# Kernel tuning notes

Measured on AMD Instinct MI355X. Metric: run time of the kernel, lower is better.

Reference implementation:

```python
import jax, jax.numpy as jnp
import numpy as np

N_GRAPHS = 256
NEG_SLOPE = 0.2


def _add_self_loops(src, dst, edge_attr, n):
    # PyG fill_value='mean': self-loop edge_attr = per-node mean of incoming edge_attr
    sums = jax.ops.segment_sum(edge_attr, dst, num_segments=n)
    cnt = jax.ops.segment_sum(jnp.ones((dst.shape[0],), edge_attr.dtype), dst, num_segments=n)
    loop_attr = sums / jnp.maximum(cnt, 1.0)[:, None]
    loop = jnp.arange(n)
    src = jnp.concatenate([src, loop])
    dst = jnp.concatenate([dst, loop])
    ea = jnp.concatenate([edge_attr, loop_attr], axis=0)
    return src, dst, ea


def _segment_softmax(scores, seg, n):
    # scores: [E, H]; softmax over edges sharing the same target node
    m = jax.ops.segment_max(scores, seg, num_segments=n)
    ex = jnp.exp(scores - m[seg])
    s = jax.ops.segment_sum(ex, seg, num_segments=n)
    return ex / jnp.maximum(s[seg], 1e-16)


def gatv2_layer(x, src, dst, ea, w_l, w_r, w_e, att, b, heads, out_ch, concat):
    n = x.shape[0]
    x_l = (x @ w_l).reshape(n, heads, out_ch)  # source transform
    x_r = (x @ w_r).reshape(n, heads, out_ch)  # target transform
    e_f = (ea @ w_e).reshape(-1, heads, out_ch)
    m = x_l[src] + x_r[dst] + e_f                               # [E, H, C]
    score = jnp.einsum('ehc,hc->eh', jax.nn.leaky_relu(m, NEG_SLOPE), att)
    alpha = _segment_softmax(score, dst, n)                      # [E, H]
    out = jax.ops.segment_sum(alpha[:, :, None] * x_l[src], dst, num_segments=n)
    if concat:
        return out.reshape(n, heads * out_ch) + b
    return out.mean(axis=1) + b


def reference(x, edge_index, edge_attr, batch,
              w_l1, w_r1, w_e1, att1, b1,
              w_l2, w_r2, w_e2, att2, b2,
              w_fc, b_fc):
    n = x.shape[0]
    src, dst, ea = _add_self_loops(edge_index[0], edge_index[1], edge_attr, n)
    h = gatv2_layer(x, src, dst, ea, w_l1, w_r1, w_e1, att1, b1, heads=2, out_ch=32, concat=True)
    h = jax.nn.relu(h)
    h = gatv2_layer(h, src, dst, ea, w_l2, w_r2, w_e2, att2, b2, heads=1, out_ch=32, concat=False)
    h = jax.nn.relu(h)
    # global mean pool over graphs
    sums = jax.ops.segment_sum(h, batch, num_segments=N_GRAPHS)
    cnt = jax.ops.segment_sum(jnp.ones((n,), h.dtype), batch, num_segments=N_GRAPHS)
    pooled = sums / jnp.maximum(cnt, 1.0)[:, None]
    return pooled @ w_fc + b_fc


def setup_inputs() -> dict:
    key = jax.random.key(0)
    ks = jax.random.split(key, 20)
    N, E, IN, H, C, ED, OUT = 100000, 1600000, 128, 2, 32, 16, 32
    s = 0.05
    return {
        'x': jax.random.normal(ks[0], (N, IN), jnp.float32),
        'edge_index': jax.random.randint(ks[1], (2, E), 0, N, jnp.int32),
        'edge_attr': jax.random.normal(ks[2], (E, ED), jnp.float32),
        'batch': jnp.sort(jax.random.randint(ks[3], (N,), 0, 256, jnp.int32)),
        'w_l1': jax.random.normal(ks[4], (IN, H * C), jnp.float32) * s,
        'w_r1': jax.random.normal(ks[5], (IN, H * C), jnp.float32) * s,
        'w_e1': jax.random.normal(ks[6], (ED, H * C), jnp.float32) * s,
        'att1': jax.random.normal(ks[7], (H, C), jnp.float32) * s,
        'b1': jnp.zeros((H * C,), jnp.float32),
        'w_l2': jax.random.normal(ks[8], (H * C, C), jnp.float32) * s,
        'w_r2': jax.random.normal(ks[9], (H * C, C), jnp.float32) * s,
        'w_e2': jax.random.normal(ks[10], (ED, C), jnp.float32) * s,
        'att2': jax.random.normal(ks[11], (1, C), jnp.float32) * s,
        'b2': jnp.zeros((C,), jnp.float32),
        'w_fc': jax.random.normal(ks[12], (C, OUT), jnp.float32) * s,
        'b_fc': jnp.zeros((OUT,), jnp.float32),
    }
```

## Files before the change

### kernel.cpp

```cpp
#include <hip/hip_runtime.h>
#include <hip/hip_bf16.h>
#include <hip/hip_fp16.h>

#define NEG_SLOPE 0.2f
#define LOG2E 1.4426950408889634f

typedef _Float16 h2v __attribute__((ext_vector_type(2)));

__global__ void deg_count_k(const int* __restrict__ dstA, int* __restrict__ deg, int E) {
  int e = blockIdx.x * blockDim.x + threadIdx.x;
  if (e < E) atomicAdd(&deg[dstA[e]], 1);
}

__global__ void scan1_k(const int* __restrict__ deg, int* __restrict__ rowptr,
                        int* __restrict__ aux, int N) {
  __shared__ int sh[256];
  int t = threadIdx.x, i = blockIdx.x * 256 + t;
  int v = (i < N) ? deg[i] : 0;
  sh[t] = v; __syncthreads();
  for (int off = 1; off < 256; off <<= 1) {
    int x = (t >= off) ? sh[t - off] : 0;
    __syncthreads();
    sh[t] += x;
    __syncthreads();
  }
  if (i < N) rowptr[i] = sh[t] - v;
  if (t == 255) aux[blockIdx.x] = sh[255];
}

__global__ void scan2_k(int* __restrict__ aux, int naux) {
  __shared__ int sh[512];
  int t = threadIdx.x;
  int v = (t < naux) ? aux[t] : 0;
  sh[t] = v; __syncthreads();
  for (int off = 1; off < 512; off <<= 1) {
    int x = (t >= off) ? sh[t - off] : 0;
    __syncthreads();
    sh[t] += x;
    __syncthreads();
  }
  if (t < naux) aux[t] = sh[t] - v;
}

__global__ void scan3_k(int* __restrict__ rowptr, int* __restrict__ cursor,
                        const int* __restrict__ aux, int N, int E) {
  int i = blockIdx.x * blockDim.x + threadIdx.x;
  if (i < N) {
    int r = rowptr[i] + aux[i >> 8];
    rowptr[i] = r;
    cursor[i] = r;
  } else if (i == N) {
    rowptr[N] = E;
  }
}

__global__ void scatter_k(const int* __restrict__ srcA, const int* __restrict__ dstA,
                          const float* __restrict__ ea, int* __restrict__ cursor,
                          int* __restrict__ csr_src, uint4* __restrict__ ea_h, int E) {
  int e = blockIdx.x * blockDim.x + threadIdx.x;
  if (e >= E) return;
  int pos = atomicAdd(&cursor[dstA[e]], 1);
  csr_src[pos] = srcA[e];
  const float* p = ea + (size_t)e * 16;
  union { __half2 h2[8]; uint4 u[2]; } cv;
#pragma unroll
  for (int k = 0; k < 8; ++k) cv.h2[k] = __floats2half2_rn(p[2 * k], p[2 * k + 1]);
  uint4* d = ea_h + (size_t)pos * 2;
  d[0] = cv.u[0];
  d[1] = cv.u[1];
}

__global__ __launch_bounds__(256) void transform1_k(
    const float* __restrict__ x, const float* __restrict__ wl, const float* __restrict__ wr,
    float* __restrict__ xl, float* __restrict__ xr, int N) {
  __shared__ float wS[128 * 128];
  __shared__ float xs[32 * 128];
  int t = threadIdx.x;
  for (int i = t; i < 128 * 64; i += 256) {
    int k = i >> 6, j = i & 63;
    wS[k * 128 + j]      = wl[i];
    wS[k * 128 + 64 + j] = wr[i];
  }
  __syncthreads();
  int tc = t & 31;
  int tr = t >> 5;
  int ntiles = (N + 31) >> 5;
  for (int tile = blockIdx.x; tile < ntiles; tile += gridDim.x) {
    int base = tile << 5;
    const float4* x4 = (const float4*)x;
    float4* xs4 = (float4*)xs;
    for (int i = t; i < 1024; i += 256) {
      int node = base + (i >> 5);
      float4 v = {0.f, 0.f, 0.f, 0.f};
      if (node < N) v = x4[(size_t)node * 32 + (i & 31)];
      xs4[i] = v;
    }
    __syncthreads();
    float4 acc0 = {0,0,0,0}, acc1 = {0,0,0,0}, acc2 = {0,0,0,0}, acc3 = {0,0,0,0};
    const float* xrow = &xs[tr * 4 * 128];
#pragma unroll 4
    for (int k = 0; k < 128; ++k) {
      float4 w4 = *(const float4*)&wS[k * 128 + tc * 4];
      float x0 = xrow[k], x1 = xrow[128 + k], x2 = xrow[256 + k], x3 = xrow[384 + k];
      acc0.x += x0 * w4.x; acc0.y += x0 * w4.y; acc0.z += x0 * w4.z; acc0.w += x0 * w4.w;
      acc1.x += x1 * w4.x; acc1.y += x1 * w4.y; acc1.z += x1 * w4.z; acc1.w += x1 * w4.w;
      acc2.x += x2 * w4.x; acc2.y += x2 * w4.y; acc2.z += x2 * w4.z; acc2.w += x2 * w4.w;
      acc3.x += x3 * w4.x; acc3.y += x3 * w4.y; acc3.z += x3 * w4.z; acc3.w += x3 * w4.w;
    }
    float* dp = (tc < 16) ? xl : xr;
    int j4 = (tc & 15) * 4;
    int nb = base + tr * 4;
    if (nb + 0 < N) *(float4*)&dp[(size_t)(nb + 0) * 64 + j4] = acc0;
    if (nb + 1 < N) *(float4*)&dp[(size_t)(nb + 1) * 64 + j4] = acc1;
    if (nb + 2 < N) *(float4*)&dp[(size_t)(nb + 2) * 64 + j4] = acc2;
    if (nb + 3 < N) *(float4*)&dp[(size_t)(nb + 3) * 64 + j4] = acc3;
    __syncthreads();
  }
}

__global__ __launch_bounds__(256) void transform2_k(
    const float* __restrict__ h, const float* __restrict__ wl, const float* __restrict__ wr,
    float* __restrict__ xl, float* __restrict__ xr, int N) {
  __shared__ float wS[64 * 64];
  __shared__ float xs[64 * 64];
  int t = threadIdx.x;
  for (int i = t; i < 64 * 32; i += 256) {
    int k = i >> 5, j = i & 31;
    wS[k * 64 + j]      = wl[i];
    wS[k * 64 + 32 + j] = wr[i];
  }
  __syncthreads();
  int tc = t & 15;
  int tr = t >> 4;
  int ntiles = (N + 63) >> 6;
  for (int tile = blockIdx.x; tile < ntiles; tile += gridDim.x) {
    int base = tile << 6;
    const float4* h4 = (const float4*)h;
    float4* xs4 = (float4*)xs;
    for (int i = t; i < 1024; i += 256) {
      int node = base + (i >> 4);
      float4 v = {0.f, 0.f, 0.f, 0.f};
      if (node < N) v = h4[(size_t)node * 16 + (i & 15)];
      xs4[i] = v;
    }
    __syncthreads();
    float4 acc0 = {0,0,0,0}, acc1 = {0,0,0,0}, acc2 = {0,0,0,0}, acc3 = {0,0,0,0};
    const float* xrow = &xs[tr * 4 * 64];
#pragma unroll 4
    for (int k = 0; k < 64; ++k) {
      float4 w4 = *(const float4*)&wS[k * 64 + tc * 4];
      float x0 = xrow[k], x1 = xrow[64 + k], x2 = xrow[128 + k], x3 = xrow[192 + k];
      acc0.x += x0 * w4.x; acc0.y += x0 * w4.y; acc0.z += x0 * w4.z; acc0.w += x0 * w4.w;
      acc1.x += x1 * w4.x; acc1.y += x1 * w4.y; acc1.z += x1 * w4.z; acc1.w += x1 * w4.w;
      acc2.x += x2 * w4.x; acc2.y += x2 * w4.y; acc2.z += x2 * w4.z; acc2.w += x2 * w4.w;
      acc3.x += x3 * w4.x; acc3.y += x3 * w4.y; acc3.z += x3 * w4.z; acc3.w += x3 * w4.w;
    }
    float* dp = (tc < 8) ? xl : xr;
    int j4 = (tc & 7) * 4;
    int nb = base + tr * 4;
    if (nb + 0 < N) *(float4*)&dp[(size_t)(nb + 0) * 32 + j4] = acc0;
    if (nb + 1 < N) *(float4*)&dp[(size_t)(nb + 1) * 32 + j4] = acc1;
    if (nb + 2 < N) *(float4*)&dp[(size_t)(nb + 2) * 32 + j4] = acc2;
    if (nb + 3 < N) *(float4*)&dp[(size_t)(nb + 3) * 32 + j4] = acc3;
    __syncthreads();
  }
}

__global__ __launch_bounds__(256) void gat1_k(
    const int* __restrict__ rowptr, const int* __restrict__ csr_src,
    const uint4* __restrict__ ea_h, const float* __restrict__ we,
    const float* __restrict__ att, const float* __restrict__ b,
    const float* __restrict__ xl, const float* __restrict__ xr,
    float* __restrict__ h, int N) {
  int t = threadIdx.x;
  int lane = t & 63;
  h2v wh[8];
#pragma unroll
  for (int k = 0; k < 8; ++k) {
    wh[k].x = (_Float16)we[(2 * k) * 64 + lane];
    wh[k].y = (_Float16)we[(2 * k + 1) * 64 + lane];
  }
  float att_r = att[lane] * LOG2E;
  float b_r = b[lane];
  int wid = (blockIdx.x * blockDim.x + t) >> 6;
  int n0 = wid * 4;
  for (int jj = 0; jj < 4; ++jj) {
    int n = n0 + jj;
    if (n >= N) break;
    float xr_v = xr[(size_t)n * 64 + lane];
    float xl_s = xl[(size_t)n * 64 + lane];
    float num = 0.f, den = 0.f, efsum = 0.f;
    int rs = __builtin_amdgcn_readfirstlane(rowptr[n]);
    int re = __builtin_amdgcn_readfirstlane(rowptr[n + 1]);
    for (int base = rs; base < re; base += 64) {
      int cnt = min(64, re - base);
      int s_l = 0;
      if (lane < cnt) s_l = csr_src[base + lane];
      int i = 0;
      for (; i + 1 < cnt; i += 2) {
        int sa = __shfl(s_l, i), sb = __shfl(s_l, i + 1);
        float xa = xl[(size_t)sa * 64 + lane];
        float xb = xl[(size_t)sb * 64 + lane];
        const uint4* epa = ea_h + (size_t)(base + i) * 2;
        union { uint4 u; h2v h[4]; } a0, a1, c0, c1;
        a0.u = epa[0]; a1.u = epa[1];
        c0.u = epa[2]; c1.u = epa[3];
        float fa0 = 0.f, fa1 = 0.f, fb0 = 0.f, fb1 = 0.f;
        fa0 = __builtin_amdgcn_fdot2(a0.h[0], wh[0], fa0, false);
        fb0 = __builtin_amdgcn_fdot2(c0.h[0], wh[0], fb0, false);
        fa1 = __builtin_amdgcn_fdot2(a0.h[1], wh[1], fa1, false);
        fb1 = __builtin_amdgcn_fdot2(c0.h[1], wh[1], fb1, false);
        fa0 = __builtin_amdgcn_fdot2(a0.h[2], wh[2], fa0, false);
        fb0 = __builtin_amdgcn_fdot2(c0.h[2], wh[2], fb0, false);
        fa1 = __builtin_amdgcn_fdot2(a0.h[3], wh[3], fa1, false);
        fb1 = __builtin_amdgcn_fdot2(c0.h[3], wh[3], fb1, false);
        fa0 = __builtin_amdgcn_fdot2(a1.h[0], wh[4], fa0, false);
        fb0 = __builtin_amdgcn_fdot2(c1.h[0], wh[4], fb0, false);
        fa1 = __builtin_amdgcn_fdot2(a1.h[1], wh[5], fa1, false);
        fb1 = __builtin_amdgcn_fdot2(c1.h[1], wh[5], fb1, false);
        fa0 = __builtin_amdgcn_fdot2(a1.h[2], wh[6], fa0, false);
        fb0 = __builtin_amdgcn_fdot2(c1.h[2], wh[6], fb0, false);
        fa1 = __builtin_amdgcn_fdot2(a1.h[3], wh[7], fa1, false);
        fb1 = __builtin_amdgcn_fdot2(c1.h[3], wh[7], fb1, false);
        float fa = fa0 + fa1, fb = fb0 + fb1;
        float ma = xa + xr_v + fa; ma = (ma > 0.f) ? ma : NEG_SLOPE * ma;
        float mb = xb + xr_v + fb; mb = (mb > 0.f) ? mb : NEG_SLOPE * mb;
        float ta = ma * att_r, tb = mb * att_r;
#pragma unroll
        for (int off = 1; off < 32; off <<= 1) {
          ta += __shfl_xor(ta, off);
          tb += __shfl_xor(tb, off);
        }
        float ga = exp2f(ta), gb = exp2f(tb);
        num += ga * xa + gb * xb;
        den += ga + gb;
        efsum += fa + fb;
      }
      if (i < cnt) {
        int sa = __shfl(s_l, i);
        float xa = xl[(size_t)sa * 64 + lane];
        const uint4* epa = ea_h + (size_t)(base + i) * 2;
        union { uint4 u; h2v h[4]; } a0, a1;
        a0.u = epa[0]; a1.u = epa[1];
        float fa0 = 0.f, fa1 = 0.f;
        fa0 = __builtin_amdgcn_fdot2(a0.h[0], wh[0], fa0, false);
        fa1 = __builtin_amdgcn_fdot2(a0.h[1], wh[1], fa1, false);
        fa0 = __builtin_amdgcn_fdot2(a0.h[2], wh[2], fa0, false);
        fa1 = __builtin_amdgcn_fdot2(a0.h[3], wh[3], fa1, false);
        fa0 = __builtin_amdgcn_fdot2(a1.h[0], wh[4], fa0, false);
        fa1 = __builtin_amdgcn_fdot2(a1.h[1], wh[5], fa1, false);
        fa0 = __builtin_amdgcn_fdot2(a1.h[2], wh[6], fa0, false);
        fa1 = __builtin_amdgcn_fdot2(a1.h[3], wh[7], fa1, false);
        float fa = fa0 + fa1;
        float ma = xa + xr_v + fa; ma = (ma > 0.f) ? ma : NEG_SLOPE * ma;
        float ta = ma * att_r;
#pragma unroll
        for (int off = 1; off < 32; off <<= 1) ta += __shfl_xor(ta, off);
        float ga = exp2f(ta);
        num += ga * xa;
        den += ga;
        efsum += fa;
      }
    }
    int deg = re - rs;
    float ef_self = efsum / fmaxf((float)deg, 1.f);
    float mm = xl_s + xr_v + ef_self;
    mm = (mm > 0.f) ? mm : NEG_SLOPE * mm;
    float s2 = mm * att_r;
#pragma unroll
    for (int off = 1; off < 32; off <<= 1) s2 += __shfl_xor(s2, off);
    float e2 = exp2f(s2);
    num += e2 * xl_s;
    den += e2;
    h[(size_t)n * 64 + lane] = fmaxf(num / fmaxf(den, 1e-16f) + b_r, 0.f);
  }
}

__global__ __launch_bounds__(256) void gat2_k(
    const int* __restrict__ rowptr, const int* __restrict__ csr_src,
    const uint4* __restrict__ ea_h, const float* __restrict__ we,
    const float* __restrict__ att, const float* __restrict__ b,
    const float* __restrict__ xl, const float* __restrict__ xr,
    float* __restrict__ h, int N) {
  int t = threadIdx.x;
  int lane = t & 63;
  int c = lane & 31;
  int half = lane >> 5;
  int hbase = lane & 32;
  h2v wh[8];
#pragma unroll
  for (int k = 0; k < 8; ++k) {
    wh[k].x = (_Float16)we[(2 * k) * 32 + c];
    wh[k].y = (_Float16)we[(2 * k + 1) * 32 + c];
  }
  float att_r = att[c] * LOG2E;
  float b_r = b[c];
  int wid = (blockIdx.x * blockDim.x + t) >> 6;
  int p0 = wid * 4;
  for (int jj = 0; jj < 4; ++jj) {
    int p = p0 + jj;
    if (p * 2 >= N) break;
    int n = p * 2 + half;
    if (n >= N) continue;
    float xr_v = xr[(size_t)n * 32 + c];
    float xl_s = xl[(size_t)n * 32 + c];
    float num = 0.f, den = 0.f, efsum = 0.f;
    int rs = rowptr[n], re = rowptr[n + 1];
    for (int base = rs; base < re; base += 32) {
      int cnt = min(32, re - base);
      int s_l = 0;
      if (c < cnt) s_l = csr_src[base + c];
      int i = 0;
      for (; i + 1 < cnt; i += 2) {
        int sa = __shfl(s_l, hbase + i), sb = __shfl(s_l, hbase + i + 1);
        float xa = xl[(size_t)sa * 32 + c];
        float xb = xl[(size_t)sb * 32 + c];
        const uint4* epa = ea_h + (size_t)(base + i) * 2;
        union { uint4 u; h2v h[4]; } a0, a1, c0, c1;
        a0.u = epa[0]; a1.u = epa[1];
        c0.u = epa[2]; c1.u = epa[3];
        float fa0 = 0.f, fa1 = 0.f, fb0 = 0.f, fb1 = 0.f;
        fa0 = __builtin_amdgcn_fdot2(a0.h[0], wh[0], fa0, false);
        fb0 = __builtin_amdgcn_fdot2(c0.h[0], wh[0], fb0, false);
        fa1 = __builtin_amdgcn_fdot2(a0.h[1], wh[1], fa1, false);
        fb1 = __builtin_amdgcn_fdot2(c0.h[1], wh[1], fb1, false);
        fa0 = __builtin_amdgcn_fdot2(a0.h[2], wh[2], fa0, false);
        fb0 = __builtin_amdgcn_fdot2(c0.h[2], wh[2], fb0, false);
        fa1 = __builtin_amdgcn_fdot2(a0.h[3], wh[3], fa1, false);
        fb1 = __builtin_amdgcn_fdot2(c0.h[3], wh[3], fb1, false);
        fa0 = __builtin_amdgcn_fdot2(a1.h[0], wh[4], fa0, false);
        fb0 = __builtin_amdgcn_fdot2(c1.h[0], wh[4], fb0, false);
        fa1 = __builtin_amdgcn_fdot2(a1.h[1], wh[5], fa1, false);
        fb1 = __builtin_amdgcn_fdot2(c1.h[1], wh[5], fb1, false);
        fa0 = __builtin_amdgcn_fdot2(a1.h[2], wh[6], fa0, false);
        fb0 = __builtin_amdgcn_fdot2(c1.h[2], wh[6], fb0, false);
        fa1 = __builtin_amdgcn_fdot2(a1.h[3], wh[7], fa1, false);
        fb1 = __builtin_amdgcn_fdot2(c1.h[3], wh[7], fb1, false);
        float fa = fa0 + fa1, fb = fb0 + fb1;
        float ma = xa + xr_v + fa; ma = (ma > 0.f) ? ma : NEG_SLOPE * ma;
        float mb = xb + xr_v + fb; mb = (mb > 0.f) ? mb : NEG_SLOPE * mb;
        float ta = ma * att_r, tb = mb * att_r;
#pragma unroll
        for (int off = 1; off < 32; off <<= 1) {
          ta += __shfl_xor(ta, off);
          tb += __shfl_xor(tb, off);
        }
        float ga = exp2f(ta), gb = exp2f(tb);
        num += ga * xa + gb * xb;
        den += ga + gb;
        efsum += fa + fb;
      }
      if (i < cnt) {
        int sa = __shfl(s_l, hbase + i);
        float xa = xl[(size_t)sa * 32 + c];
        const uint4* epa = ea_h + (size_t)(base + i) * 2;
        union { uint4 u; h2v h[4]; } a0, a1;
        a0.u = epa[0]; a1.u = epa[1];
        float fa0 = 0.f, fa1 = 0.f;
        fa0 = __builtin_amdgcn_fdot2(a0.h[0], wh[0], fa0, false);
        fa1 = __builtin_amdgcn_fdot2(a0.h[1], wh[1], fa1, false);
        fa0 = __builtin_amdgcn_fdot2(a0.h[2], wh[2], fa0, false);
        fa1 = __builtin_amdgcn_fdot2(a0.h[3], wh[3], fa1, false);
        fa0 = __builtin_amdgcn_fdot2(a1.h[0], wh[4], fa0, false);
        fa1 = __builtin_amdgcn_fdot2(a1.h[1], wh[5], fa1, false);
        fa0 = __builtin_amdgcn_fdot2(a1.h[2], wh[6], fa0, false);
        fa1 = __builtin_amdgcn_fdot2(a1.h[3], wh[7], fa1, false);
        float fa = fa0 + fa1;
        float ma = xa + xr_v + fa; ma = (ma > 0.f) ? ma : NEG_SLOPE * ma;
        float ta = ma * att_r;
#pragma unroll
        for (int off = 1; off < 32; off <<= 1) ta += __shfl_xor(ta, off);
        float ga = exp2f(ta);
        num += ga * xa;
        den += ga;
        efsum += fa;
      }
    }
    int deg = re - rs;
    float ef_self = efsum / fmaxf((float)deg, 1.f);
    float mm = xl_s + xr_v + ef_self;
    mm = (mm > 0.f) ? mm : NEG_SLOPE * mm;
    float s2 = mm * att_r;
#pragma unroll
    for (int off = 1; off < 32; off <<= 1) s2 += __shfl_xor(s2, off);
    float e2 = exp2f(s2);
    num += e2 * xl_s;
    den += e2;
    h[(size_t)n * 32 + c] = fmaxf(num / fmaxf(den, 1e-16f) + b_r, 0.f);
  }
}

__global__ __launch_bounds__(256) void pool_fc_k(
    const float* __restrict__ h, const int* __restrict__ batch,
    const float* __restrict__ wfc, const float* __restrict__ bfc,
    float* __restrict__ out, int N) {
  int g = blockIdx.x;
  __shared__ int srange[2];
  __shared__ float part[8][32];
  int t = threadIdx.x;
  if (t < 2) {
    int key = g + t;
    int lo = 0, hi = N;
    while (lo < hi) { int mid = (lo + hi) >> 1; if (batch[mid] < key) lo = mid + 1; else hi = mid; }
    srange[t] = lo;
  }
  __syncthreads();
  int rs = srange[0], re = srange[1];
  int c = t & 31, sub = t >> 5;
  float acc = 0.f;
  for (int n = rs + sub; n < re; n += 8) acc += h[(size_t)n * 32 + c];
  part[sub][c] = acc;
  __syncthreads();
  if (sub == 0) {
    float s = part[0][c];
#pragma unroll
    for (int i = 1; i < 8; ++i) s += part[i][c];
    part[0][c] = s / fmaxf((float)(re - rs), 1.f);
  }
  __syncthreads();
  if (sub == 0) {
    float a = 0.f;
#pragma unroll
    for (int k = 0; k < 32; ++k) a += part[0][k] * wfc[k * 32 + c];
    out[g * 32 + c] = a + bfc[c];
  }
}

extern "C" void kernel_launch(void* const* d_in, const int* in_sizes, int n_in,
                              void* d_out, int out_size, void* d_ws, size_t ws_size,
                              hipStream_t stream) {
  const float* x   = (const float*)d_in[0];
  const int*   ei  = (const int*)d_in[1];
  const float* ea  = (const float*)d_in[2];
  const int*   bat = (const int*)d_in[3];
  const float* wl1 = (const float*)d_in[4];
  const float* wr1 = (const float*)d_in[5];
  const float* we1 = (const float*)d_in[6];
  const float* at1 = (const float*)d_in[7];
  const float* b1  = (const float*)d_in[8];
  const float* wl2 = (const float*)d_in[9];
  const float* wr2 = (const float*)d_in[10];
  const float* we2 = (const float*)d_in[11];
  const float* at2 = (const float*)d_in[12];
  const float* b2  = (const float*)d_in[13];
  const float* wfc = (const float*)d_in[14];
  const float* bfc = (const float*)d_in[15];

  const int N = in_sizes[0] / 128;
  const int E = in_sizes[1] / 2;
  const int G = 256;
  const int* srcA = ei;
  const int* dstA = ei + E;

  uint4* ea_h   = (uint4*)d_ws;
  float* xl1    = (float*)(ea_h + (size_t)E * 2);
  float* xr1    = xl1 + (size_t)N * 64;
  int*   deg    = (int*)(xr1 + (size_t)N * 64);
  int*   rowptr = deg + N;
  int*   cursor = rowptr + (N + 1);
  int*   aux    = cursor + N;
  int*   csr_src= aux + 512;
  float* h1     = xr1;
  float* xl2    = xl1;
  float* xr2    = xl1 + (size_t)N * 32;
  float* h2     = xr2;

  const int naux = (N + 255) / 256;

  hipMemsetAsync(deg, 0, (size_t)N * sizeof(int), stream);
  deg_count_k<<<(E + 255) / 256, 256, 0, stream>>>(dstA, deg, E);
  scan1_k<<<naux, 256, 0, stream>>>(deg, rowptr, aux, N);
  scan2_k<<<1, 512, 0, stream>>>(aux, naux);
  scan3_k<<<(N + 256) / 256, 256, 0, stream>>>(rowptr, cursor, aux, N, E);
  scatter_k<<<(E + 255) / 256, 256, 0, stream>>>(srcA, dstA, ea, cursor, csr_src, ea_h, E);

  transform1_k<<<(N + 31) / 32, 256, 0, stream>>>(x, wl1, wr1, xl1, xr1, N);
  {
    int blocks1 = (N + 15) / 16;
    gat1_k<<<blocks1, 256, 0, stream>>>(rowptr, csr_src, ea_h, we1, at1, b1,
                                        xl1, xr1, h1, N);
  }

  transform2_k<<<(N + 63) / 64, 256, 0, stream>>>(h1, wl2, wr2, xl2, xr2, N);
  {
    int P = (N + 1) / 2;
    int blocks2 = (P + 15) / 16;
    gat2_k<<<blocks2, 256, 0, stream>>>(rowptr, csr_src, ea_h, we2, at2, b2,
                                        xl2, xr2, h2, N);
  }

  pool_fc_k<<<G, 256, 0, stream>>>(h2, bat, wfc, bfc, (float*)d_out, N);
}
```

Baseline: 530.0 us.

## Process one node per wave in layer-2 GAT with edges split across half-waves

The second GAT layer now assigns a whole wave to each node, with the two 32-lane halves handling alternating edges and merging partial sums by cross-half shuffle. Source indices are broadcast with readlane instead of shuffle, row bounds are made wave-uniform, and leaky-relu becomes a fmaxf form in both layers. This aims to remove divergence from degree imbalance between two nodes sharing a wave, at the cost of twice as many waves and duplicated per-node epilogue work.

```diff
diff --git a/kernel.cpp b/kernel.cpp
--- a/kernel.cpp
+++ b/kernel.cpp
@@ -198,9 +198,12 @@
       if (lane < cnt) s_l = csr_src[base + lane];
       int i = 0;
       for (; i + 1 < cnt; i += 2) {
-        int sa = __shfl(s_l, i), sb = __shfl(s_l, i + 1);
-        float xa = xl[(size_t)sa * 64 + lane];
-        float xb = xl[(size_t)sb * 64 + lane];
+        int sa = __builtin_amdgcn_readlane(s_l, i);
+        int sb = __builtin_amdgcn_readlane(s_l, i + 1);
+        const float* pa = xl + (size_t)sa * 64;
+        const float* pb = xl + (size_t)sb * 64;
+        float xa = pa[lane];
+        float xb = pb[lane];
         const uint4* epa = ea_h + (size_t)(base + i) * 2;
         union { uint4 u; h2v h[4]; } a0, a1, c0, c1;
         a0.u = epa[0]; a1.u = epa[1];
@@ -223,8 +226,8 @@
         fa1 = __builtin_amdgcn_fdot2(a1.h[3], wh[7], fa1, false);
         fb1 = __builtin_amdgcn_fdot2(c1.h[3], wh[7], fb1, false);
         float fa = fa0 + fa1, fb = fb0 + fb1;
-        float ma = xa + xr_v + fa; ma = (ma > 0.f) ? ma : NEG_SLOPE * ma;
-        float mb = xb + xr_v + fb; mb = (mb > 0.f) ? mb : NEG_SLOPE * mb;
+        float ma = xa + xr_v + fa; ma = fmaxf(ma, NEG_SLOPE * ma);
+        float mb = xb + xr_v + fb; mb = fmaxf(mb, NEG_SLOPE * mb);
         float ta = ma * att_r, tb = mb * att_r;
 #pragma unroll
         for (int off = 1; off < 32; off <<= 1) {
@@ -237,8 +240,9 @@
         efsum += fa + fb;
       }
       if (i < cnt) {
-        int sa = __shfl(s_l, i);
-        float xa = xl[(size_t)sa * 64 + lane];
+        int sa = __builtin_amdgcn_readlane(s_l, i);
+        const float* pa = xl + (size_t)sa * 64;
+        float xa = pa[lane];
         const uint4* epa = ea_h + (size_t)(base + i) * 2;
         union { uint4 u; h2v h[4]; } a0, a1;
         a0.u = epa[0]; a1.u = epa[1];
@@ -252,7 +256,7 @@
         fa0 = __builtin_amdgcn_fdot2(a1.h[2], wh[6], fa0, false);
         fa1 = __builtin_amdgcn_fdot2(a1.h[3], wh[7], fa1, false);
         float fa = fa0 + fa1;
-        float ma = xa + xr_v + fa; ma = (ma > 0.f) ? ma : NEG_SLOPE * ma;
+        float ma = xa + xr_v + fa; ma = fmaxf(ma, NEG_SLOPE * ma);
         float ta = ma * att_r;
 #pragma unroll
         for (int off = 1; off < 32; off <<= 1) ta += __shfl_xor(ta, off);
@@ -265,7 +269,7 @@
     int deg = re - rs;
     float ef_self = efsum / fmaxf((float)deg, 1.f);
     float mm = xl_s + xr_v + ef_self;
-    mm = (mm > 0.f) ? mm : NEG_SLOPE * mm;
+    mm = fmaxf(mm, NEG_SLOPE * mm);
     float s2 = mm * att_r;
 #pragma unroll
     for (int off = 1; off < 32; off <<= 1) s2 += __shfl_xor(s2, off);
@@ -285,8 +289,7 @@
   int t = threadIdx.x;
   int lane = t & 63;
   int c = lane & 31;
-  int half = lane >> 5;
-  int hbase = lane & 32;
+  int par = lane >> 5;
   h2v wh[8];
 #pragma unroll
   for (int k = 0; k < 8; ++k) {
@@ -296,66 +299,29 @@
   float att_r = att[c] * LOG2E;
   float b_r = b[c];
   int wid = (blockIdx.x * blockDim.x + t) >> 6;
-  int p0 = wid * 4;
+  int n0 = wid * 4;
   for (int jj = 0; jj < 4; ++jj) {
-    int p = p0 + jj;
-    if (p * 2 >= N) break;
-    int n = p * 2 + half;
-    if (n >= N) continue;
+    int n = n0 + jj;
+    if (n >= N) break;
     float xr_v = xr[(size_t)n * 32 + c];
     float xl_s = xl[(size_t)n * 32 + c];
     float num = 0.f, den = 0.f, efsum = 0.f;
-    int rs = rowptr[n], re = rowptr[n + 1];
-    for (int base = rs; base < re; base += 32) {
-      int cnt = min(32, re - base);
+    int rs = __builtin_amdgcn_readfirstlane(rowptr[n]);
+    int re = __builtin_amdgcn_readfirstlane(rowptr[n + 1]);
+    for (int base = rs; base < re; base += 64) {
+      int cnt = min(64, re - base);
       int s_l = 0;
-      if (c < cnt) s_l = csr_src[base + c];
+      if (lane < cnt) s_l = csr_src[base + lane];
       int i = 0;
       for (; i + 1 < cnt; i += 2) {
-        int sa = __shfl(s_l, hbase + i), sb = __shfl(s_l, hbase + i + 1);
-        float xa = xl[(size_t)sa * 32 + c];
-        float xb = xl[(size_t)sb * 32 + c];
-        const uint4* epa = ea_h + (size_t)(base + i) * 2;
-        union { uint4 u; h2v h[4]; } a0, a1, c0, c1;
-        a0.u = epa[0]; a1.u = epa[1];
-        c0.u = epa[2]; c1.u = epa[3];
-        float fa0 = 0.f, fa1 = 0.f, fb0 = 0.f, fb1 = 0.f;
-        fa0 = __builtin_amdgcn_fdot2(a0.h[0], wh[0], fa0, false);
-        fb0 = __builtin_amdgcn_fdot2(c0.h[0], wh[0], fb0, false);
-        fa1 = __builtin_amdgcn_fdot2(a0.h[1], wh[1], fa1, false);
-        fb1 = __builtin_amdgcn_fdot2(c0.h[1], wh[1], fb1, false);
-        fa0 = __builtin_amdgcn_fdot2(a0.h[2], wh[2], fa0, false);
-        fb0 = __builtin_amdgcn_fdot2(c0.h[2], wh[2], fb0, false);
-        fa1 = __builtin_amdgcn_fdot2(a0.h[3], wh[3], fa1, false);
-        fb1 = __builtin_amdgcn_fdot2(c0.h[3], wh[3], fb1, false);
-        fa0 = __builtin_amdgcn_fdot2(a1.h[0], wh[4], fa0, false);
-        fb0 = __builtin_amdgcn_fdot2(c1.h[0], wh[4], fb0, false);
-        fa1 = __builtin_amdgcn_fdot2(a1.h[1], wh[5], fa1, false);
-        fb1 = __builtin_amdgcn_fdot2(c1.h[1], wh[5], fb1, false);
-        fa0 = __builtin_amdgcn_fdot2(a1.h[2], wh[6], fa0, false);
-        fb0 = __builtin_amdgcn_fdot2(c1.h[2], wh[6], fb0, false);
-        fa1 = __builtin_amdgcn_fdot2(a1.h[3], wh[7], fa1, false);
-        fb1 = __builtin_amdgcn_fdot2(c1.h[3], wh[7], fb1, false);
-        float fa = fa0 + fa1, fb = fb0 + fb1;
-        float ma = xa + xr_v + fa; ma = (ma > 0.f) ? ma : NEG_SLOPE * ma;
-        float mb = xb + xr_v + fb; mb = (mb > 0.f) ? mb : NEG_SLOPE * mb;
-        float ta = ma * att_r, tb = mb * att_r;
-#pragma unroll
-        for (int off = 1; off < 32; off <<= 1) {
-          ta += __shfl_xor(ta, off);
-          tb += __shfl_xor(tb, off);
-        }
-        float ga = exp2f(ta), gb = exp2f(tb);
-        num += ga * xa + gb * xb;
-        den += ga + gb;
-        efsum += fa + fb;
-      }
-      if (i < cnt) {
-        int sa = __shfl(s_l, hbase + i);
-        float xa = xl[(size_t)sa * 32 + c];
-        const uint4* epa = ea_h + (size_t)(base + i) * 2;
+        int sa0 = __builtin_amdgcn_readlane(s_l, i);
+        int sa1 = __builtin_amdgcn_readlane(s_l, i + 1);
+        int sa = par ? sa1 : sa0;
+        const float* p = xl + (size_t)sa * 32;
+        float xa = p[c];
+        const uint4* ep = ea_h + (size_t)(base + i + par) * 2;
         union { uint4 u; h2v h[4]; } a0, a1;
-        a0.u = epa[0]; a1.u = epa[1];
+        a0.u = ep[0]; a1.u = ep[1];
         float fa0 = 0.f, fa1 = 0.f;
         fa0 = __builtin_amdgcn_fdot2(a0.h[0], wh[0], fa0, false);
         fa1 = __builtin_amdgcn_fdot2(a0.h[1], wh[1], fa1, false);
@@ -366,7 +332,7 @@
         fa0 = __builtin_amdgcn_fdot2(a1.h[2], wh[6], fa0, false);
         fa1 = __builtin_amdgcn_fdot2(a1.h[3], wh[7], fa1, false);
         float fa = fa0 + fa1;
-        float ma = xa + xr_v + fa; ma = (ma > 0.f) ? ma : NEG_SLOPE * ma;
+        float ma = xa + xr_v + fa; ma = fmaxf(ma, NEG_SLOPE * ma);
         float ta = ma * att_r;
 #pragma unroll
         for (int off = 1; off < 32; off <<= 1) ta += __shfl_xor(ta, off);
@@ -375,18 +341,49 @@
         den += ga;
         efsum += fa;
       }
-    }
+      if (i < cnt) {
+        if (par == 0) {
+          int sa = __builtin_amdgcn_readlane(s_l, i);
+          const float* p = xl + (size_t)sa * 32;
+          float xa = p[c];
+          const uint4* ep = ea_h + (size_t)(base + i) * 2;
+          union { uint4 u; h2v h[4]; } a0, a1;
+          a0.u = ep[0]; a1.u = ep[1];
+          float fa0 = 0.f, fa1 = 0.f;
+          fa0 = __builtin_amdgcn_fdot2(a0.h[0], wh[0], fa0, false);
+          fa1 = __builtin_amdgcn_fdot2(a0.h[1], wh[1], fa1, false);
+          fa0 = __builtin_amdgcn_fdot2(a0.h[2], wh[2], fa0, false);
+          fa1 = __builtin_amdgcn_fdot2(a0.h[3], wh[3], fa1, false);
+          fa0 = __builtin_amdgcn_fdot2(a1.h[0], wh[4], fa0, false);
+          fa1 = __builtin_amdgcn_fdot2(a1.h[1], wh[5], fa1, false);
+          fa0 = __builtin_amdgcn_fdot2(a1.h[2], wh[6], fa0, false);
+          fa1 = __builtin_amdgcn_fdot2(a1.h[3], wh[7], fa1, false);
+          float fa = fa0 + fa1;
+          float ma = xa + xr_v + fa; ma = fmaxf(ma, NEG_SLOPE * ma);
+          float ta = ma * att_r;
+#pragma unroll
+          for (int off = 1; off < 32; off <<= 1) ta += __shfl_xor(ta, off);
+          float ga = exp2f(ta);
+          num += ga * xa;
+          den += ga;
+          efsum += fa;
+        }
+      }
+    }
+    num += __shfl_xor(num, 32);
+    den += __shfl_xor(den, 32);
+    efsum += __shfl_xor(efsum, 32);
     int deg = re - rs;
     float ef_self = efsum / fmaxf((float)deg, 1.f);
     float mm = xl_s + xr_v + ef_self;
-    mm = (mm > 0.f) ? mm : NEG_SLOPE * mm;
+    mm = fmaxf(mm, NEG_SLOPE * mm);
     float s2 = mm * att_r;
 #pragma unroll
     for (int off = 1; off < 32; off <<= 1) s2 += __shfl_xor(s2, off);
     float e2 = exp2f(s2);
     num += e2 * xl_s;
     den += e2;
-    h[(size_t)n * 32 + c] = fmaxf(num / fmaxf(den, 1e-16f) + b_r, 0.f);
+    if (par == 0) h[(size_t)n * 32 + c] = fmaxf(num / fmaxf(den, 1e-16f) + b_r, 0.f);
   }
 }
 
@@ -483,8 +480,7 @@
 
   transform2_k<<<(N + 63) / 64, 256, 0, stream>>>(h1, wl2, wr2, xl2, xr2, N);
   {
-    int P = (N + 1) / 2;
-    int blocks2 = (P + 15) / 16;
+    int blocks2 = (N + 15) / 16;
     gat2_k<<<blocks2, 256, 0, stream>>>(rowptr, csr_src, ea_h, we2, at2, b2,
                                         xl2, xr2, h2, N);
   }
```

Result: no change. 540.4 us (+2.0%).

## Fuse degree counting into layer-1 transform launch and use fast math intrinsics

Applied to the files above, without the earlier changes.

Merges the edge-degree atomic counting kernel into the first-layer feature transform kernel as extra blocks, so both run in one launch and can overlap. The transform now runs before the CSR build instead of after scatter. The GAT kernels switch to readlane for broadcasting source indices, fmax-based leaky ReLU, hardware exp2, and reciprocal instead of division. These changes cut launch overhead and ALU cost, but the transform blocks reserve large shared memory, which may limit occupancy for the atomic blocks.

```diff
diff --git a/kernel.cpp b/kernel.cpp
--- a/kernel.cpp
+++ b/kernel.cpp
@@ -6,11 +6,6 @@
 #define LOG2E 1.4426950408889634f
 
 typedef _Float16 h2v __attribute__((ext_vector_type(2)));
-
-__global__ void deg_count_k(const int* __restrict__ dstA, int* __restrict__ deg, int E) {
-  int e = blockIdx.x * blockDim.x + threadIdx.x;
-  if (e < E) atomicAdd(&deg[dstA[e]], 1);
-}
 
 __global__ void scan1_k(const int* __restrict__ deg, int* __restrict__ rowptr,
                         int* __restrict__ aux, int N) {
@@ -70,12 +65,23 @@
   d[1] = cv.u[1];
 }
 
-__global__ __launch_bounds__(256) void transform1_k(
+__global__ __launch_bounds__(256) void t1deg_k(
     const float* __restrict__ x, const float* __restrict__ wl, const float* __restrict__ wr,
-    float* __restrict__ xl, float* __restrict__ xr, int N) {
+    float* __restrict__ xl, float* __restrict__ xr, int N,
+    const int* __restrict__ dstA, int* __restrict__ deg, int E, int degBlocks) {
   __shared__ float wS[128 * 128];
   __shared__ float xs[32 * 128];
   int t = threadIdx.x;
+  if ((int)blockIdx.x < degBlocks) {
+    int base = blockIdx.x * 1024 + t;
+#pragma unroll
+    for (int k = 0; k < 4; ++k) {
+      int e = base + k * 256;
+      if (e < E) atomicAdd(&deg[dstA[e]], 1);
+    }
+    return;
+  }
+  int tile = blockIdx.x - degBlocks;
   for (int i = t; i < 128 * 64; i += 256) {
     int k = i >> 6, j = i & 63;
     wS[k * 128 + j]      = wl[i];
@@ -84,8 +90,7 @@
   __syncthreads();
   int tc = t & 31;
   int tr = t >> 5;
-  int ntiles = (N + 31) >> 5;
-  for (int tile = blockIdx.x; tile < ntiles; tile += gridDim.x) {
+  {
     int base = tile << 5;
     const float4* x4 = (const float4*)x;
     float4* xs4 = (float4*)xs;
@@ -114,7 +119,6 @@
     if (nb + 1 < N) *(float4*)&dp[(size_t)(nb + 1) * 64 + j4] = acc1;
     if (nb + 2 < N) *(float4*)&dp[(size_t)(nb + 2) * 64 + j4] = acc2;
     if (nb + 3 < N) *(float4*)&dp[(size_t)(nb + 3) * 64 + j4] = acc3;
-    __syncthreads();
   }
 }
 
@@ -198,9 +202,12 @@
       if (lane < cnt) s_l = csr_src[base + lane];
       int i = 0;
       for (; i + 1 < cnt; i += 2) {
-        int sa = __shfl(s_l, i), sb = __shfl(s_l, i + 1);
-        float xa = xl[(size_t)sa * 64 + lane];
-        float xb = xl[(size_t)sb * 64 + lane];
+        int sa = __builtin_amdgcn_readlane(s_l, i);
+        int sb = __builtin_amdgcn_readlane(s_l, i + 1);
+        const float* pa = xl + (size_t)sa * 64;
+        const float* pb = xl + (size_t)sb * 64;
+        float xa = pa[lane];
+        float xb = pb[lane];
         const uint4* epa = ea_h + (size_t)(base + i) * 2;
         union { uint4 u; h2v h[4]; } a0, a1, c0, c1;
         a0.u = epa[0]; a1.u = epa[1];
@@ -223,22 +230,23 @@
         fa1 = __builtin_amdgcn_fdot2(a1.h[3], wh[7], fa1, false);
         fb1 = __builtin_amdgcn_fdot2(c1.h[3], wh[7], fb1, false);
         float fa = fa0 + fa1, fb = fb0 + fb1;
-        float ma = xa + xr_v + fa; ma = (ma > 0.f) ? ma : NEG_SLOPE * ma;
-        float mb = xb + xr_v + fb; mb = (mb > 0.f) ? mb : NEG_SLOPE * mb;
+        float ma = xa + xr_v + fa; ma = fmaxf(ma, NEG_SLOPE * ma);
+        float mb = xb + xr_v + fb; mb = fmaxf(mb, NEG_SLOPE * mb);
         float ta = ma * att_r, tb = mb * att_r;
 #pragma unroll
         for (int off = 1; off < 32; off <<= 1) {
           ta += __shfl_xor(ta, off);
           tb += __shfl_xor(tb, off);
         }
-        float ga = exp2f(ta), gb = exp2f(tb);
+        float ga = __builtin_amdgcn_exp2f(ta), gb = __builtin_amdgcn_exp2f(tb);
         num += ga * xa + gb * xb;
         den += ga + gb;
         efsum += fa + fb;
       }
       if (i < cnt) {
-        int sa = __shfl(s_l, i);
-        float xa = xl[(size_t)sa * 64 + lane];
+        int sa = __builtin_amdgcn_readlane(s_l, i);
+        const float* pa = xl + (size_t)sa * 64;
+        float xa = pa[lane];
         const uint4* epa = ea_h + (size_t)(base + i) * 2;
         union { uint4 u; h2v h[4]; } a0, a1;
         a0.u = epa[0]; a1.u = epa[1];
@@ -252,27 +260,27 @@
         fa0 = __builtin_amdgcn_fdot2(a1.h[2], wh[6], fa0, false);
         fa1 = __builtin_amdgcn_fdot2(a1.h[3], wh[7], fa1, false);
         float fa = fa0 + fa1;
-        float ma = xa + xr_v + fa; ma = (ma > 0.f) ? ma : NEG_SLOPE * ma;
+        float ma = xa + xr_v + fa; ma = fmaxf(ma, NEG_SLOPE * ma);
         float ta = ma * att_r;
 #pragma unroll
         for (int off = 1; off < 32; off <<= 1) ta += __shfl_xor(ta, off);
-        float ga = exp2f(ta);
+        float ga = __builtin_amdgcn_exp2f(ta);
         num += ga * xa;
         den += ga;
         efsum += fa;
       }
     }
     int deg = re - rs;
-    float ef_self = efsum / fmaxf((float)deg, 1.f);
+    float ef_self = efsum * __builtin_amdgcn_rcpf(fmaxf((float)deg, 1.f));
     float mm = xl_s + xr_v + ef_self;
-    mm = (mm > 0.f) ? mm : NEG_SLOPE * mm;
+    mm = fmaxf(mm, NEG_SLOPE * mm);
     float s2 = mm * att_r;
 #pragma unroll
     for (int off = 1; off < 32; off <<= 1) s2 += __shfl_xor(s2, off);
-    float e2 = exp2f(s2);
+    float e2 = __builtin_amdgcn_exp2f(s2);
     num += e2 * xl_s;
     den += e2;
-    h[(size_t)n * 64 + lane] = fmaxf(num / fmaxf(den, 1e-16f) + b_r, 0.f);
+    h[(size_t)n * 64 + lane] = fmaxf(num * __builtin_amdgcn_rcpf(fmaxf(den, 1e-16f)) + b_r, 0.f);
   }
 }
 
@@ -337,15 +345,15 @@
         fa1 = __builtin_amdgcn_fdot2(a1.h[3], wh[7], fa1, false);
         fb1 = __builtin_amdgcn_fdot2(c1.h[3], wh[7], fb1, false);
         float fa = fa0 + fa1, fb = fb0 + fb1;
-        float ma = xa + xr_v + fa; ma = (ma > 0.f) ? ma : NEG_SLOPE * ma;
-        float mb = xb + xr_v + fb; mb = (mb > 0.f) ? mb : NEG_SLOPE * mb;
+        float ma = xa + xr_v + fa; ma = fmaxf(ma, NEG_SLOPE * ma);
+        float mb = xb + xr_v + fb; mb = fmaxf(mb, NEG_SLOPE * mb);
         float ta = ma * att_r, tb = mb * att_r;
 #pragma unroll
         for (int off = 1; off < 32; off <<= 1) {
           ta += __shfl_xor(ta, off);
           tb += __shfl_xor(tb, off);
         }
-        float ga = exp2f(ta), gb = exp2f(tb);
+        float ga = __builtin_amdgcn_exp2f(ta), gb = __builtin_amdgcn_exp2f(tb);
         num += ga * xa + gb * xb;
         den += ga + gb;
         efsum += fa + fb;
@@ -366,27 +374,27 @@
         fa0 = __builtin_amdgcn_fdot2(a1.h[2], wh[6], fa0, false);
         fa1 = __builtin_amdgcn_fdot2(a1.h[3], wh[7], fa1, false);
         float fa = fa0 + fa1;
-        float ma = xa + xr_v + fa; ma = (ma > 0.f) ? ma : NEG_SLOPE * ma;
+        float ma = xa + xr_v + fa; ma = fmaxf(ma, NEG_SLOPE * ma);
         float ta = ma * att_r;
 #pragma unroll
         for (int off = 1; off < 32; off <<= 1) ta += __shfl_xor(ta, off);
-        float ga = exp2f(ta);
+        float ga = __builtin_amdgcn_exp2f(ta);
         num += ga * xa;
         den += ga;
         efsum += fa;
       }
     }
     int deg = re - rs;
-    float ef_self = efsum / fmaxf((float)deg, 1.f);
+    float ef_self = efsum * __builtin_amdgcn_rcpf(fmaxf((float)deg, 1.f));
     float mm = xl_s + xr_v + ef_self;
-    mm = (mm > 0.f) ? mm : NEG_SLOPE * mm;
+    mm = fmaxf(mm, NEG_SLOPE * mm);
     float s2 = mm * att_r;
 #pragma unroll
     for (int off = 1; off < 32; off <<= 1) s2 += __shfl_xor(s2, off);
-    float e2 = exp2f(s2);
+    float e2 = __builtin_amdgcn_exp2f(s2);
     num += e2 * xl_s;
     den += e2;
-    h[(size_t)n * 32 + c] = fmaxf(num / fmaxf(den, 1e-16f) + b_r, 0.f);
+    h[(size_t)n * 32 + c] = fmaxf(num * __builtin_amdgcn_rcpf(fmaxf(den, 1e-16f)) + b_r, 0.f);
   }
 }
 
@@ -466,15 +474,17 @@
   float* h2     = xr2;
 
   const int naux = (N + 255) / 256;
+  const int degBlocks = (E + 1023) / 1024;
+  const int ntiles1 = (N + 31) / 32;
 
   hipMemsetAsync(deg, 0, (size_t)N * sizeof(int), stream);
-  deg_count_k<<<(E + 255) / 256, 256, 0, stream>>>(dstA, deg, E);
+  t1deg_k<<<degBlocks + ntiles1, 256, 0, stream>>>(x, wl1, wr1, xl1, xr1, N,
+                                                   dstA, deg, E, degBlocks);
   scan1_k<<<naux, 256, 0, stream>>>(deg, rowptr, aux, N);
   scan2_k<<<1, 512, 0, stream>>>(aux, naux);
   scan3_k<<<(N + 256) / 256, 256, 0, stream>>>(rowptr, cursor, aux, N, E);
   scatter_k<<<(E + 255) / 256, 256, 0, stream>>>(srcA, dstA, ea, cursor, csr_src, ea_h, E);
 
-  transform1_k<<<(N + 31) / 32, 256, 0, stream>>>(x, wl1, wr1, xl1, xr1, N);
   {
     int blocks1 = (N + 15) / 16;
     gat1_k<<<blocks1, 256, 0, stream>>>(rowptr, csr_src, ea_h, we1, at1, b1,
```

Result: faster. 513.5 us (-3.1%).
